# Kernel tuning notes

Hardware: AMD Instinct MI355X
Metric: run time of the kernel (lower is better)

The kernel has to match this reference:

```python
import jax, jax.numpy as jnp
import numpy as np

H = 8
LN_EPS = 1e-5


def _layer_norm(t):
    # LayerNorm over last dim, no affine (elementwise_affine=False, bias=False)
    mu = jnp.mean(t, axis=-1, keepdims=True)
    var = jnp.var(t, axis=-1, keepdims=True)
    return (t - mu) / jnp.sqrt(var + LN_EPS)


def setup_inputs() -> dict:
    key = jax.random.key(0)
    ks = jax.random.split(key, 7)
    B, N, D, K = 2, 8192, 512, 32
    x = jax.random.normal(ks[0], (B, N, D), dtype=jnp.float32)
    idx = jax.random.randint(ks[1], (N, K), 0, N)
    s = 1.0 / np.sqrt(D)  # kaiming-ish init scale for stability
    Wq = jax.random.normal(ks[2], (D, D), dtype=jnp.float32) * s
    Wk = jax.random.normal(ks[3], (D, D), dtype=jnp.float32) * s
    Wv = jax.random.normal(ks[4], (D, D), dtype=jnp.float32) * s
    Wout = jax.random.normal(ks[5], (D, D), dtype=jnp.float32) * s
    bout = jnp.zeros((D,), dtype=jnp.float32)
    return {"x": x, "idx": idx, "Wq": Wq, "Wk": Wk, "Wv": Wv, "Wout": Wout, "bout": bout}


def reference(x, idx, Wq, Wk, Wv, Wout, bout):
    B, N, D = x.shape
    d_k = D // H

    def proj(W):
        # torch Linear: x @ W.T ; reshape to (B, H, N, d_k)
        return (x @ W.T).reshape(B, N, H, d_k).transpose(0, 2, 1, 3)

    Q, K, V = proj(Wq), proj(Wk), proj(Wv)
    # per-head LayerNorm on d_k (all heads identical since no affine params)
    Q = _layer_norm(Q)
    K = _layer_norm(K)

    # grouped (neighborhood) attention: gather K,V at neighbor indices
    Kg = K[:, :, idx]  # (B, H, N, k, d_k)
    Vg = V[:, :, idx]  # (B, H, N, k, d_k)
    scores = jnp.einsum('bhnd,bhnkd->bhnk', Q, Kg) / jnp.sqrt(jnp.asarray(d_k, x.dtype))
    attn = jax.nn.softmax(scores, axis=-1)
    out = jnp.einsum('bhnk,bhnkd->bhnd', attn, Vg)  # (B, H, N, d_k)

    out = out.transpose(0, 2, 1, 3).reshape(B, N, D)
    return out @ Wout.T + bout
```

## Files before the change

### kernel.cpp

```cpp
#include <hip/hip_runtime.h>
#include <hip/hip_bf16.h>
#include <math.h>

#define BB 2
#define NN 8192
#define DD 512
#define HH 8
#define DK 64
#define KNB 32
#define BN (BB*NN)
#define BHN (BB*HH*NN)

typedef __attribute__((ext_vector_type(8))) _Float16 f16x8;
typedef __attribute__((ext_vector_type(2))) _Float16 f16x2;
typedef __attribute__((ext_vector_type(4))) float f32x4;

#if __has_builtin(__builtin_amdgcn_fdot2)
#define HAS_FDOT2 1
#endif

__device__ __forceinline__ unsigned short f2h(float f) {
    return __builtin_bit_cast(unsigned short, (_Float16)f);
}
__device__ __forceinline__ f16x2 u2h2(unsigned u) {
    return __builtin_bit_cast(f16x2, u);
}
__device__ __forceinline__ float h2f_lo(unsigned u) {
    return (float)__builtin_bit_cast(_Float16, (unsigned short)(u & 0xffffu));
}
__device__ __forceinline__ float h2f_hi(unsigned u) {
    return (float)__builtin_bit_cast(_Float16, (unsigned short)(u >> 16));
}
__device__ __forceinline__ float dot2h(unsigned a, unsigned b, float c) {
#ifdef HAS_FDOT2
    return __builtin_amdgcn_fdot2(u2h2(a), u2h2(b), c, false);
#else
    c = fmaf(h2f_lo(a), h2f_lo(b), c);
    return fmaf(h2f_hi(a), h2f_hi(b), c);
#endif
}

__device__ __forceinline__ void gload_lds16(const void* gptr, void* lptr) {
    __builtin_amdgcn_global_load_lds(
        (const __attribute__((address_space(1))) unsigned int*)gptr,
        (__attribute__((address_space(3))) unsigned int*)lptr,
        16, 0, 0);
}
__device__ __forceinline__ void gload_lds4(const void* gptr, void* lptr) {
    __builtin_amdgcn_global_load_lds(
        (const __attribute__((address_space(1))) unsigned int*)gptr,
        (__attribute__((address_space(3))) unsigned int*)lptr,
        4, 0, 0);
}

__global__ __launch_bounds__(256) void cvt_all(
    const float* __restrict__ x,
    const float* __restrict__ Wq, const float* __restrict__ Wk,
    const float* __restrict__ Wv, const float* __restrict__ Wo,
    unsigned short* __restrict__ Xb, unsigned short* __restrict__ Wfb,
    unsigned short* __restrict__ Wob)
{
    const int blk = blockIdx.x;
    const float* src;
    unsigned short* dst;
    int off;
    if (blk < 8192) {
        off = (blk * 256 + threadIdx.x) * 4;
        src = x; dst = Xb;
    } else {
        const int e = ((blk - 8192) * 256 + threadIdx.x) * 4;
        const int t = e >> 18;
        off = e & 262143;
        src = (t == 0) ? Wq : (t == 1) ? Wk : (t == 2) ? Wv : Wo;
        dst = (t < 3) ? (Wfb + (size_t)t * 262144) : Wob;
    }
    const float4 v = *(const float4*)(src + off);
    ushort4 u;
    u.x = f2h(v.x); u.y = f2h(v.y); u.z = f2h(v.z); u.w = f2h(v.w);
    *(ushort4*)(dst + off) = u;
}

__global__ __launch_bounds__(256) void gemm_qkv(
    const unsigned short* __restrict__ Xb, const unsigned short* __restrict__ Wfb,
    unsigned short* __restrict__ Qh, unsigned short* __restrict__ Kh,
    unsigned short* __restrict__ Vh)
{
    __shared__ unsigned short Als[128 * 32];
    __shared__ unsigned short Bls[128 * 32];
    const int tid  = threadIdx.x;
    const int wave = tid >> 6, lane = tid & 63;
    const int wm = wave >> 1, wn = wave & 1;
    const int quad = lane >> 4, r = lane & 15;
    const int row0 = blockIdx.x * 128;
    const int c0   = blockIdx.y * 128;

    f32x4 acc[4][4];
    #pragma unroll
    for (int i = 0; i < 4; ++i)
        #pragma unroll
        for (int j = 0; j < 4; ++j) acc[i][j] = (f32x4)0.f;

    const char* Ab = (const char*)Xb;
    const char* Bb = (const char*)Wfb;

    for (int k0 = 0; k0 < 512; k0 += 32) {
        __syncthreads();
        #pragma unroll
        for (int q = 0; q < 2; ++q) {
            const int li = q * 4096 + wave * 1024 + lane * 16;
            const int rr = li >> 6, off = li & 63;
            gload_lds16(Ab + (size_t)(row0 + rr) * 1024 + k0 * 2 + off,
                        (char*)Als + (q * 4096 + wave * 1024));
            gload_lds16(Bb + (size_t)(c0 + rr) * 1024 + k0 * 2 + off,
                        (char*)Bls + (q * 4096 + wave * 1024));
        }
        __syncthreads();

        f16x8 af[4], bf[4];
        #pragma unroll
        for (int i = 0; i < 4; ++i)
            af[i] = *(const f16x8*)(&Als[(wm * 64 + i * 16 + r) * 32 + quad * 8]);
        #pragma unroll
        for (int j = 0; j < 4; ++j)
            bf[j] = *(const f16x8*)(&Bls[(wn * 64 + j * 16 + r) * 32 + quad * 8]);
        #pragma unroll
        for (int i = 0; i < 4; ++i)
            #pragma unroll
            for (int j = 0; j < 4; ++j)
                acc[i][j] = __builtin_amdgcn_mfma_f32_16x16x32_f16(af[i], bf[j], acc[i][j], 0, 0, 0);
    }

    const int tensor = c0 >> 9;
    unsigned short* OutH = (tensor == 0) ? Qh : (tensor == 1) ? Kh : Vh;

    float mu[4][4], rs[4][4];
    if (tensor < 2) {
        #pragma unroll
        for (int i = 0; i < 4; ++i) {
            #pragma unroll
            for (int reg = 0; reg < 4; ++reg) {
                float sm = acc[i][0][reg] + acc[i][1][reg] + acc[i][2][reg] + acc[i][3][reg];
                sm += __shfl_xor(sm, 1); sm += __shfl_xor(sm, 2);
                sm += __shfl_xor(sm, 4); sm += __shfl_xor(sm, 8);
                const float muv = sm * (1.f / 64.f);
                float qv = 0.f;
                #pragma unroll
                for (int j = 0; j < 4; ++j) {
                    const float dv = acc[i][j][reg] - muv;
                    qv = fmaf(dv, dv, qv);
                }
                qv += __shfl_xor(qv, 1); qv += __shfl_xor(qv, 2);
                qv += __shfl_xor(qv, 4); qv += __shfl_xor(qv, 8);
                mu[i][reg] = muv;
                rs[i][reg] = rsqrtf(qv * (1.f / 64.f) + 1e-5f);
            }
        }
    }

    #pragma unroll
    for (int i = 0; i < 4; ++i) {
        #pragma unroll
        for (int j = 0; j < 4; ++j) {
            const int cc = (c0 & 511) + wn * 64 + j * 16 + r;
            const int h = cc >> 6, d = cc & 63;
            #pragma unroll
            for (int reg = 0; reg < 4; ++reg) {
                const int row = row0 + wm * 64 + i * 16 + quad * 4 + reg;
                const int b = row >> 13, n = row & 8191;
                float v = acc[i][j][reg];
                if (tensor < 2) v = (v - mu[i][reg]) * rs[i][reg];
                OutH[(((size_t)(b * HH + h) * NN + n) << 6) + d] = f2h(v);
            }
        }
    }
}

__global__ __launch_bounds__(256, 2) void attn(
    const unsigned short* __restrict__ Qh, const unsigned short* __restrict__ Kh,
    const unsigned short* __restrict__ Vh,
    const int* __restrict__ idx, unsigned short* __restrict__ Ob)
{
    __shared__ unsigned short Vls[4][2048];
    const int p = blockIdx.x;
    const int L = ((p & 7) << 12) | (p >> 3);
    const int wave = threadIdx.x >> 6;
    const int wid  = L * 4 + wave;
    const int lane = threadIdx.x & 63;
    const int bh = wid >> 13;
    const int n  = wid & 8191;
    const size_t base = (size_t)bh * NN * DK;

    const int k    = lane >> 1;
    const int half = lane & 1;
    const int g    = idx[n * KNB + k];

    const unsigned gg = (unsigned)g | (((unsigned)__shfl_xor(g, 2)) << 16);

    char* lw = (char*)Vls[wave];
    const char* Vbytes = (const char*)Vh + (base << 1);
    const int col4 = (lane & 31) * 4;
    const int sub  = lane >> 5;
    #pragma unroll
    for (int j = 0; j < 16; ++j) {
        const unsigned gpair = (unsigned)__builtin_amdgcn_readlane((int)gg, j * 4);
        const int grow = sub ? (int)(gpair >> 16) : (int)(gpair & 0xffffu);
        gload_lds4(Vbytes + grow * 128 + col4, lw + j * 256);
    }

    const uint4* q4 = (const uint4*)(Qh + base + ((size_t)n << 6) + half * 32);
    const uint4* k4 = (const uint4*)(Kh + base + ((size_t)g << 6) + half * 32);
    float acc = 0.f;
    #pragma unroll
    for (int c = 0; c < 4; ++c) {
        const uint4 qa = q4[c], ka = k4[c];
        acc = dot2h(qa.x, ka.x, acc);
        acc = dot2h(qa.y, ka.y, acc);
        acc = dot2h(qa.z, ka.z, acc);
        acc = dot2h(qa.w, ka.w, acc);
    }
    float s = (acc + __shfl_xor(acc, 1)) * 0.125f;

    float m = s;
    #pragma unroll
    for (int off = 2; off <= 32; off <<= 1) m = fmaxf(m, __shfl_xor(m, off));
    const float e = __expf(s - m);
    float tot = e;
    #pragma unroll
    for (int off = 2; off <= 32; off <<= 1) tot += __shfl_xor(tot, off);
    const float pr = e / tot;

    const unsigned prh = (unsigned)f2h(pr);
    const unsigned pp = prh | (((unsigned)__shfl_xor((int)prh, 2)) << 16);

    __syncthreads();
    const unsigned short* lv = (const unsigned short*)Vls[wave];
    float o = 0.f;
    #pragma unroll
    for (int j = 0; j < 16; ++j) {
        const unsigned ppair = (unsigned)__builtin_amdgcn_readlane((int)pp, j * 4);
        const unsigned v0 = lv[j * 128 + lane];
        const unsigned v1 = lv[j * 128 + 64 + lane];
        o = dot2h(v0 | (v1 << 16), ppair, o);
    }
    const int b = bh >> 3, h = bh & 7;
    Ob[((size_t)(b * NN + n)) * DD + h * DK + lane] = f2h(o);
}

__global__ __launch_bounds__(256) void gemm_out(
    const unsigned short* __restrict__ Ob, const unsigned short* __restrict__ Wob,
    const float* __restrict__ bout, float* __restrict__ out)
{
    __shared__ unsigned short Als[128 * 32];
    __shared__ unsigned short Bls[128 * 32];
    const int tid  = threadIdx.x;
    const int wave = tid >> 6, lane = tid & 63;
    const int wm = wave >> 1, wn = wave & 1;
    const int quad = lane >> 4, r = lane & 15;
    const int row0 = blockIdx.x * 128;
    const int c0   = blockIdx.y * 128;

    f32x4 acc[4][4];
    #pragma unroll
    for (int i = 0; i < 4; ++i)
        #pragma unroll
        for (int j = 0; j < 4; ++j) acc[i][j] = (f32x4)0.f;

    const char* Ab = (const char*)Ob;
    const char* Bb = (const char*)Wob;

    for (int k0 = 0; k0 < 512; k0 += 32) {
        __syncthreads();
        #pragma unroll
        for (int q = 0; q < 2; ++q) {
            const int li = q * 4096 + wave * 1024 + lane * 16;
            const int rr = li >> 6, off = li & 63;
            gload_lds16(Ab + (size_t)(row0 + rr) * 1024 + k0 * 2 + off,
                        (char*)Als + (q * 4096 + wave * 1024));
            gload_lds16(Bb + (size_t)(c0 + rr) * 1024 + k0 * 2 + off,
                        (char*)Bls + (q * 4096 + wave * 1024));
        }
        __syncthreads();

        f16x8 af[4], bf[4];
        #pragma unroll
        for (int i = 0; i < 4; ++i)
            af[i] = *(const f16x8*)(&Als[(wm * 64 + i * 16 + r) * 32 + quad * 8]);
        #pragma unroll
        for (int j = 0; j < 4; ++j)
            bf[j] = *(const f16x8*)(&Bls[(wn * 64 + j * 16 + r) * 32 + quad * 8]);
        #pragma unroll
        for (int i = 0; i < 4; ++i)
            #pragma unroll
            for (int j = 0; j < 4; ++j)
                acc[i][j] = __builtin_amdgcn_mfma_f32_16x16x32_f16(af[i], bf[j], acc[i][j], 0, 0, 0);
    }

    #pragma unroll
    for (int i = 0; i < 4; ++i) {
        #pragma unroll
        for (int j = 0; j < 4; ++j) {
            const int colg = c0 + wn * 64 + j * 16 + r;
            const float bb = bout[colg];
            #pragma unroll
            for (int reg = 0; reg < 4; ++reg) {
                const int row = row0 + wm * 64 + i * 16 + quad * 4 + reg;
                out[((size_t)row << 9) + colg] = acc[i][j][reg] + bb;
            }
        }
    }
}

extern "C" void kernel_launch(void* const* d_in, const int* in_sizes, int n_in,
                              void* d_out, int out_size, void* d_ws, size_t ws_size,
                              hipStream_t stream)
{
    const float* x    = (const float*)d_in[0];
    const int*   idx  = (const int*)  d_in[1];
    const float* Wq   = (const float*)d_in[2];
    const float* Wk   = (const float*)d_in[3];
    const float* Wv   = (const float*)d_in[4];
    const float* Wout = (const float*)d_in[5];
    const float* bout = (const float*)d_in[6];

    char* ws = (char*)d_ws;
    unsigned short* Qh  = (unsigned short*)(ws);
    unsigned short* Kh  = (unsigned short*)(ws + 16777216);
    unsigned short* Vh  = (unsigned short*)(ws + 33554432);
    unsigned short* Xb  = (unsigned short*)(ws + 50331648);
    unsigned short* Ob  = Xb;
    unsigned short* Wfb = (unsigned short*)(ws + 67108864);
    unsigned short* Wob = (unsigned short*)(ws + 68681728);
    float* out = (float*)d_out;

    cvt_all<<<9216, 256, 0, stream>>>(x, Wq, Wk, Wv, Wout, Xb, Wfb, Wob);

    dim3 g1(BN / 128, 1536 / 128);
    gemm_qkv<<<g1, 256, 0, stream>>>(Xb, Wfb, Qh, Kh, Vh);

    attn<<<BHN / 4, 256, 0, stream>>>(Qh, Kh, Vh, idx, Ob);

    dim3 g2(BN / 128, 512 / 128);
    gemm_out<<<g2, 256, 0, stream>>>(Ob, Wob, bout, out);
}
```

Baseline: 230.4 us.

## Gather V rows with 16-byte LDS loads and split PV across wave halves

The V gather into LDS now uses four 16-byte global_load_lds per lane instead of sixteen 4-byte ones, with neighbor indices distributed via ds_bpermute. The block-wide __syncthreads is replaced by a per-wave vmcnt wait, since each wave reads only its own LDS slice. The PV reduction splits the 32 neighbors between the two half-waves: each lane computes two output columns with byte permutes, the halves are combined by a shuffle, and the result is stored as a packed pair. The aim is fewer load instructions and less synchronization, at the cost of extra bpermute traffic and reliance on the vmcnt wait covering the LDS-direct loads.

```diff
diff --git a/kernel.cpp b/kernel.cpp
--- a/kernel.cpp
+++ b/kernel.cpp
@@ -45,12 +45,6 @@
         (const __attribute__((address_space(1))) unsigned int*)gptr,
         (__attribute__((address_space(3))) unsigned int*)lptr,
         16, 0, 0);
-}
-__device__ __forceinline__ void gload_lds4(const void* gptr, void* lptr) {
-    __builtin_amdgcn_global_load_lds(
-        (const __attribute__((address_space(1))) unsigned int*)gptr,
-        (__attribute__((address_space(3))) unsigned int*)lptr,
-        4, 0, 0);
 }
 
 __global__ __launch_bounds__(256) void cvt_all(
@@ -190,22 +184,21 @@
     const int n  = wid & 8191;
     const size_t base = (size_t)bh * NN * DK;
 
+    const int g_all = idx[n * KNB + (lane & 31)];
+
+    char* lw = (char*)Vls[wave];
+    const char* Vbytes = (const char*)Vh + (base << 1);
+    const int col16 = (lane & 7) * 16;
+    const int pa = (lane >> 3) * 4;
+    #pragma unroll
+    for (int j = 0; j < 4; ++j) {
+        const int gv = __builtin_amdgcn_ds_bpermute(pa + j * 32, g_all);
+        gload_lds16(Vbytes + (size_t)(gv * 128) + col16, lw + j * 1024);
+    }
+
     const int k    = lane >> 1;
     const int half = lane & 1;
-    const int g    = idx[n * KNB + k];
-
-    const unsigned gg = (unsigned)g | (((unsigned)__shfl_xor(g, 2)) << 16);
-
-    char* lw = (char*)Vls[wave];
-    const char* Vbytes = (const char*)Vh + (base << 1);
-    const int col4 = (lane & 31) * 4;
-    const int sub  = lane >> 5;
-    #pragma unroll
-    for (int j = 0; j < 16; ++j) {
-        const unsigned gpair = (unsigned)__builtin_amdgcn_readlane((int)gg, j * 4);
-        const int grow = sub ? (int)(gpair >> 16) : (int)(gpair & 0xffffu);
-        gload_lds4(Vbytes + grow * 128 + col4, lw + j * 256);
-    }
+    const int g    = __builtin_amdgcn_ds_bpermute(k * 4, g_all);
 
     const uint4* q4 = (const uint4*)(Qh + base + ((size_t)n << 6) + half * 32);
     const uint4* k4 = (const uint4*)(Kh + base + ((size_t)g << 6) + half * 32);
@@ -232,18 +225,28 @@
     const unsigned prh = (unsigned)f2h(pr);
     const unsigned pp = prh | (((unsigned)__shfl_xor((int)prh, 2)) << 16);
 
-    __syncthreads();
-    const unsigned short* lv = (const unsigned short*)Vls[wave];
-    float o = 0.f;
-    #pragma unroll
-    for (int j = 0; j < 16; ++j) {
-        const unsigned ppair = (unsigned)__builtin_amdgcn_readlane((int)pp, j * 4);
-        const unsigned v0 = lv[j * 128 + lane];
-        const unsigned v1 = lv[j * 128 + 64 + lane];
-        o = dot2h(v0 | (v1 << 16), ppair, o);
-    }
-    const int b = bh >> 3, h = bh & 7;
-    Ob[((size_t)(b * NN + n)) * DD + h * DK + lane] = f2h(o);
+    asm volatile("s_waitcnt vmcnt(0)" ::: "memory");
+
+    const int c2 = lane & 31, h2 = lane >> 5;
+    const char* lb = lw + h2 * 2048 + c2 * 4;
+    float o0 = 0.f, o1 = 0.f;
+    #pragma unroll
+    for (int j = 0; j < 8; ++j) {
+        const unsigned vx = *(const unsigned*)(lb + j * 256);
+        const unsigned vy = *(const unsigned*)(lb + j * 256 + 128);
+        const unsigned ppj = (unsigned)__builtin_amdgcn_ds_bpermute(h2 * 128 + j * 16, (int)pp);
+        const unsigned t0 = __builtin_amdgcn_perm(vx, vy, 0x01000504u);
+        const unsigned t1 = __builtin_amdgcn_perm(vx, vy, 0x03020706u);
+        o0 = dot2h(t0, ppj, o0);
+        o1 = dot2h(t1, ppj, o1);
+    }
+    o0 += __shfl_xor(o0, 32);
+    o1 += __shfl_xor(o1, 32);
+    if (lane < 32) {
+        const int b = bh >> 3, hh = bh & 7;
+        const unsigned ov = (unsigned)f2h(o0) | ((unsigned)f2h(o1) << 16);
+        *(unsigned*)(Ob + ((size_t)(b * NN + n)) * DD + hh * DK + 2 * c2) = ov;
+    }
 }
 
 __global__ __launch_bounds__(256) void gemm_out(
```

New measurement: 221.7 us. 3.7% less time.
